# Kernel tuning notes

Measured on AMD Instinct MI355X. Metric: run time of the kernel, lower is better.

Reference implementation:

```python
import jax, jax.numpy as jnp
import numpy as np

N = 8192   # samples
D = 128    # number of variables / towers (dims[0])
D1 = 128   # hidden width (dims[1])


def setup_inputs() -> dict:
    key = jax.random.key(0)
    k_x, k_w0, k_w1, k_b1 = jax.random.split(key, 4)
    x = jax.random.normal(k_x, (N, D), dtype=jnp.float32)
    # Layer 0: one Linear(D -> D1) per tower -> batched weight [D_towers, D1, D_in]
    W0 = jax.random.normal(k_w0, (D, D1, D), dtype=jnp.float32) * (1.0 / np.sqrt(D))
    # NOTEARS init: zero self-edge column i of tower i, zero layer-0 biases
    idx = jnp.arange(D)
    W0 = W0.at[idx, :, idx].set(0.0)
    b0 = jnp.zeros((D, D1), dtype=jnp.float32)
    # Layer 1: Linear(D1 -> 1) per tower
    W1 = jax.random.normal(k_w1, (D, 1, D1), dtype=jnp.float32) * (1.0 / np.sqrt(D1))
    b1 = jax.random.normal(k_b1, (D, 1), dtype=jnp.float32) * 0.05
    return {"x": x, "W0": W0, "b0": b0, "W1": W1, "b1": b1}


def reference(x, W0, b0, W1, b1):
    # binary-input check from the original forward
    binary = jnp.all((x == 0) | (x == 1))
    # Layer 0 for all D towers at once: [n,d] x [k,h,d] -> [n,k,h]
    h = jax.nn.sigmoid(jnp.einsum('nd,khd->nkh', x, W0) + b0)
    # Layer 1 (output dim 1 per tower): [n,k,h] x [k,h] -> [n,k]
    out = jnp.einsum('nkh,kh->nk', h, W1[:, 0, :]) + b1[:, 0]
    out = jnp.where(binary, jax.nn.sigmoid(out), out)
    return out
```

## Files before the change

kernel.cpp:

```cpp
#include <hip/hip_runtime.h>
#include <hip/hip_bf16.h>
#include <stdint.h>

#define N_SAMP 8192
#define D_TOW  128
#define D_HID  128

typedef __bf16 bf16x8 __attribute__((ext_vector_type(8)));
typedef float  f32x4  __attribute__((ext_vector_type(4)));

__device__ __forceinline__ ushort f2bf(float f) {
  union { float f; uint32_t u; } c; c.f = f;
  uint32_t u = c.u;
  return (ushort)((u + 0x7FFFu + ((u >> 16) & 1u)) >> 16);
}

__device__ __forceinline__ float fast_sigmoid(float p) {
  float e = __builtin_amdgcn_exp2f(p * -1.442695040888963f);
  return __builtin_amdgcn_rcpf(1.0f + e);
}

__global__ __launch_bounds__(256) void prep_kernel(
    const float* __restrict__ x, const float* __restrict__ w0,
    ushort* __restrict__ xb, ushort* __restrict__ w0b, int* __restrict__ flag) {
  const int NX4 = (N_SAMP * D_TOW) / 4;
  const int NW4 = (D_TOW * D_HID * D_TOW) / 4;
  int t = blockIdx.x * blockDim.x + threadIdx.x;
  if (t < NX4) {
    float4 v = ((const float4*)x)[t];
    bool bad = !(((v.x == 0.f) || (v.x == 1.f)) &&
                 ((v.y == 0.f) || (v.y == 1.f)) &&
                 ((v.z == 0.f) || (v.z == 1.f)) &&
                 ((v.w == 0.f) || (v.w == 1.f)));
    ushort4 o;
    o.x = f2bf(v.x); o.y = f2bf(v.y); o.z = f2bf(v.z); o.w = f2bf(v.w);
    ((ushort4*)xb)[t] = o;
    if (__ballot(bad) != 0ull && (threadIdx.x & 63) == 0) *flag = 1;
  } else if (t < NX4 + NW4) {
    int j = t - NX4;
    float4 v = ((const float4*)w0)[j];
    ushort4 o;
    o.x = f2bf(v.x); o.y = f2bf(v.y); o.z = f2bf(v.z); o.w = f2bf(v.w);
    ((ushort4*)w0b)[j] = o;
  }
}

__device__ __forceinline__ void g2l16(const void* g, void* l) {
  __builtin_amdgcn_global_load_lds(
      (const __attribute__((address_space(1))) void*)g,
      (__attribute__((address_space(3))) void*)l, 16, 0, 0);
}

__global__ __launch_bounds__(256, 2) void towers_kernel(
    const ushort* __restrict__ xb, const ushort* __restrict__ w0b,
    const float* __restrict__ b0, const float* __restrict__ w1,
    const float* __restrict__ b1, const int* __restrict__ flag,
    float* __restrict__ out) {
  __shared__ __align__(16) ushort sX[128 * 128];
  __shared__ __align__(16) ushort sW[128 * 128];
  __shared__ float sRed[128][2];

  int bid = blockIdx.x;
  int xcd = bid & 7;
  int idx = bid >> 3;
  int k = xcd * 16 + (idx >> 6);
  int n0 = (idx & 63) * 128;

  int tid = threadIdx.x;
  int lane = tid & 63;
  int wave = tid >> 6;
  int q = lane >> 4;
  int cl = lane & 15;

  const ushort* xg = xb + n0 * 128;
  const ushort* wg = w0b + k * (128 * 128);

#pragma unroll
  for (int i = 0; i < 8; ++i) {
    int base = wave * 8192 + i * 1024;
    int row = wave * 32 + i * 4 + q;
    int c = cl ^ (row & 15);
    int off = row * 128 + c * 8;
    g2l16(xg + off, (char*)sX + base);
    g2l16(wg + off, (char*)sW + base);
  }
  __syncthreads();

  int R  = (wave >> 1) * 64;
  int Ch = (wave & 1) * 64;

  f32x4 acc[4][4];
#pragma unroll
  for (int hf = 0; hf < 4; ++hf)
#pragma unroll
    for (int nf = 0; nf < 4; ++nf)
      acc[hf][nf] = (f32x4){0.f, 0.f, 0.f, 0.f};

  int aBase[4], bBase[4];
#pragma unroll
  for (int f = 0; f < 4; ++f) {
    aBase[f] = (Ch + f * 16 + cl) * 256;
    bBase[f] = (R + f * 16 + cl) * 256;
  }

#pragma unroll
  for (int t = 0; t < 4; ++t) {
    int ch = ((t * 4 + q) ^ cl) << 4;
    bf16x8 a[4], b[4];
#pragma unroll
    for (int hf = 0; hf < 4; ++hf)
      a[hf] = *(const bf16x8*)((const char*)sW + aBase[hf] + ch);
#pragma unroll
    for (int nf = 0; nf < 4; ++nf)
      b[nf] = *(const bf16x8*)((const char*)sX + bBase[nf] + ch);
#pragma unroll
    for (int hf = 0; hf < 4; ++hf)
#pragma unroll
      for (int nf = 0; nf < 4; ++nf)
        acc[hf][nf] = __builtin_amdgcn_mfma_f32_16x16x32_bf16(
            a[hf], b[nf], acc[hf][nf], 0, 0, 0);
  }

  f32x4 bb[4], wv[4];
#pragma unroll
  for (int hf = 0; hf < 4; ++hf) {
    int h = k * 128 + Ch + hf * 16 + q * 4;
    bb[hf] = *(const f32x4*)&b0[h];
    wv[hf] = *(const f32x4*)&w1[h];
  }
  float s[4] = {0.f, 0.f, 0.f, 0.f};
#pragma unroll
  for (int hf = 0; hf < 4; ++hf)
#pragma unroll
    for (int nf = 0; nf < 4; ++nf)
#pragma unroll
      for (int r = 0; r < 4; ++r)
        s[nf] += wv[hf][r] * fast_sigmoid(acc[hf][nf][r] + bb[hf][r]);

#pragma unroll
  for (int m = 16; m <= 32; m <<= 1)
#pragma unroll
    for (int nf = 0; nf < 4; ++nf)
      s[nf] += __shfl_xor(s[nf], m, 64);

  if (q == 0) {
#pragma unroll
    for (int nf = 0; nf < 4; ++nf)
      sRed[R + nf * 16 + cl][wave & 1] = s[nf];
  }
  __syncthreads();

  if (tid < 128) {
    float v = sRed[tid][0] + sRed[tid][1] + b1[k];
    if (*flag == 0) v = fast_sigmoid(v);
    out[(size_t)(n0 + tid) * D_TOW + k] = v;
  }
}

extern "C" void kernel_launch(void* const* d_in, const int* in_sizes, int n_in,
                              void* d_out, int out_size, void* d_ws, size_t ws_size,
                              hipStream_t stream) {
  const float* x  = (const float*)d_in[0];
  const float* w0 = (const float*)d_in[1];
  const float* b0 = (const float*)d_in[2];
  const float* w1 = (const float*)d_in[3];
  const float* b1 = (const float*)d_in[4];
  float* out = (float*)d_out;

  char* ws = (char*)d_ws;
  int* flag = (int*)ws;
  ushort* xb  = (ushort*)(ws + 1024);
  ushort* w0b = (ushort*)(ws + 1024 + N_SAMP * D_TOW * 2);

  hipMemsetAsync(flag, 0, 4, stream);

  int total4 = (N_SAMP * D_TOW + D_TOW * D_HID * D_TOW) / 4;
  prep_kernel<<<total4 / 256, 256, 0, stream>>>(x, w0, xb, w0b, flag);

  towers_kernel<<<8192, 256, 0, stream>>>(xb, w0b, b0, w1, b1, flag, out);
}
```

Baseline: 138.0 us.

## Drop X LDS staging, raise occupancy, fold exp scale into weights, per-block flags

The tower kernel no longer stages x tiles in LDS. It reads B fragments straight from global memory, which halves shared memory use, and launch bounds are raised to 4 blocks per SIMD. The -log2(e) factor is folded into W0 during bf16 conversion and into b0, and the sigmoid now shares one reciprocal across each pair of values. The binary check writes a flag per block instead of using a memset plus one global flag, removing a launch, and the tile order now iterates k fastest for W reuse. In exchange, the direct global loads of x may be less efficient, and the pair-shared reciprocal slightly changes the numerics.

```diff
diff --git a/kernel.cpp b/kernel.cpp
--- a/kernel.cpp
+++ b/kernel.cpp
@@ -22,11 +22,15 @@
 
 __global__ __launch_bounds__(256) void prep_kernel(
     const float* __restrict__ x, const float* __restrict__ w0,
-    ushort* __restrict__ xb, ushort* __restrict__ w0b, int* __restrict__ flag) {
+    ushort* __restrict__ xb, ushort* __restrict__ w0b,
+    int* __restrict__ flagArr) {
   const int NX4 = (N_SAMP * D_TOW) / 4;
-  const int NW4 = (D_TOW * D_HID * D_TOW) / 4;
-  int t = blockIdx.x * blockDim.x + threadIdx.x;
-  if (t < NX4) {
+  int bid = blockIdx.x;
+  int tid = threadIdx.x;
+  int t = bid * 256 + tid;
+  if (bid < 1024) {
+    __shared__ int sbad;
+    if (tid == 0) sbad = 0;
     float4 v = ((const float4*)x)[t];
     bool bad = !(((v.x == 0.f) || (v.x == 1.f)) &&
                  ((v.y == 0.f) || (v.y == 1.f)) &&
@@ -35,12 +39,17 @@
     ushort4 o;
     o.x = f2bf(v.x); o.y = f2bf(v.y); o.z = f2bf(v.z); o.w = f2bf(v.w);
     ((ushort4*)xb)[t] = o;
-    if (__ballot(bad) != 0ull && (threadIdx.x & 63) == 0) *flag = 1;
-  } else if (t < NX4 + NW4) {
+    __syncthreads();
+    if (__ballot(bad) != 0ull && (tid & 63) == 0) sbad = 1;
+    __syncthreads();
+    if (tid == 0) flagArr[bid] = sbad;
+  } else {
+    const float c = -1.442695040888963f;
     int j = t - NX4;
     float4 v = ((const float4*)w0)[j];
     ushort4 o;
-    o.x = f2bf(v.x); o.y = f2bf(v.y); o.z = f2bf(v.z); o.w = f2bf(v.w);
+    o.x = f2bf(c * v.x); o.y = f2bf(c * v.y);
+    o.z = f2bf(c * v.z); o.w = f2bf(c * v.w);
     ((ushort4*)w0b)[j] = o;
   }
 }
@@ -51,20 +60,20 @@
       (__attribute__((address_space(3))) void*)l, 16, 0, 0);
 }
 
-__global__ __launch_bounds__(256, 2) void towers_kernel(
+__global__ __launch_bounds__(256, 4) void towers_kernel(
     const ushort* __restrict__ xb, const ushort* __restrict__ w0b,
     const float* __restrict__ b0, const float* __restrict__ w1,
-    const float* __restrict__ b1, const int* __restrict__ flag,
+    const float* __restrict__ b1, const int* __restrict__ flagArr,
     float* __restrict__ out) {
-  __shared__ __align__(16) ushort sX[128 * 128];
   __shared__ __align__(16) ushort sW[128 * 128];
   __shared__ float sRed[128][2];
+  __shared__ int sBadW[4];
 
   int bid = blockIdx.x;
   int xcd = bid & 7;
   int idx = bid >> 3;
-  int k = xcd * 16 + (idx >> 6);
-  int n0 = (idx & 63) * 128;
+  int k  = xcd * 16 + (idx & 15);
+  int n0 = (idx >> 4) * 128;
 
   int tid = threadIdx.x;
   int lane = tid & 63;
@@ -72,7 +81,6 @@
   int q = lane >> 4;
   int cl = lane & 15;
 
-  const ushort* xg = xb + n0 * 128;
   const ushort* wg = w0b + k * (128 * 128);
 
 #pragma unroll
@@ -80,10 +88,14 @@
     int base = wave * 8192 + i * 1024;
     int row = wave * 32 + i * 4 + q;
     int c = cl ^ (row & 15);
-    int off = row * 128 + c * 8;
-    g2l16(xg + off, (char*)sX + base);
-    g2l16(wg + off, (char*)sW + base);
-  }
+    g2l16(wg + row * 128 + c * 8, (char*)sW + base);
+  }
+
+  int4 fv = ((const int4*)flagArr)[tid];
+  int anyb = fv.x | fv.y | fv.z | fv.w;
+  unsigned long long mb = __ballot(anyb != 0);
+  if (lane == 0) sBadW[wave] = (mb != 0ull) ? 1 : 0;
+
   __syncthreads();
 
   int R  = (wave >> 1) * 64;
@@ -96,23 +108,24 @@
     for (int nf = 0; nf < 4; ++nf)
       acc[hf][nf] = (f32x4){0.f, 0.f, 0.f, 0.f};
 
-  int aBase[4], bBase[4];
+  int aBase[4], bOff[4];
+  const char* xgc = (const char*)(xb + n0 * 128);
 #pragma unroll
   for (int f = 0; f < 4; ++f) {
     aBase[f] = (Ch + f * 16 + cl) * 256;
-    bBase[f] = (R + f * 16 + cl) * 256;
+    bOff[f]  = (R + f * 16 + cl) * 256 + q * 16;
   }
 
 #pragma unroll
   for (int t = 0; t < 4; ++t) {
+    bf16x8 a[4], b[4];
+#pragma unroll
+    for (int nf = 0; nf < 4; ++nf)
+      b[nf] = *(const bf16x8*)(xgc + bOff[nf] + t * 64);
     int ch = ((t * 4 + q) ^ cl) << 4;
-    bf16x8 a[4], b[4];
 #pragma unroll
     for (int hf = 0; hf < 4; ++hf)
       a[hf] = *(const bf16x8*)((const char*)sW + aBase[hf] + ch);
-#pragma unroll
-    for (int nf = 0; nf < 4; ++nf)
-      b[nf] = *(const bf16x8*)((const char*)sX + bBase[nf] + ch);
 #pragma unroll
     for (int hf = 0; hf < 4; ++hf)
 #pragma unroll
@@ -121,21 +134,31 @@
             a[hf], b[nf], acc[hf][nf], 0, 0, 0);
   }
 
-  f32x4 bb[4], wv[4];
+  f32x4 bbs[4], wv[4];
 #pragma unroll
   for (int hf = 0; hf < 4; ++hf) {
     int h = k * 128 + Ch + hf * 16 + q * 4;
-    bb[hf] = *(const f32x4*)&b0[h];
+    f32x4 b0v = *(const f32x4*)&b0[h];
     wv[hf] = *(const f32x4*)&w1[h];
+    bbs[hf] = b0v * -1.442695040888963f;
   }
   float s[4] = {0.f, 0.f, 0.f, 0.f};
 #pragma unroll
   for (int hf = 0; hf < 4; ++hf)
 #pragma unroll
-    for (int nf = 0; nf < 4; ++nf)
-#pragma unroll
-      for (int r = 0; r < 4; ++r)
-        s[nf] += wv[hf][r] * fast_sigmoid(acc[hf][nf][r] + bb[hf][r]);
+    for (int nf = 0; nf < 4; ++nf) {
+      f32x4 qv = acc[hf][nf] + bbs[hf];
+      float d0 = 1.0f + __builtin_amdgcn_exp2f(qv[0]);
+      float d1 = 1.0f + __builtin_amdgcn_exp2f(qv[1]);
+      float d2 = 1.0f + __builtin_amdgcn_exp2f(qv[2]);
+      float d3 = 1.0f + __builtin_amdgcn_exp2f(qv[3]);
+      float r01 = __builtin_amdgcn_rcpf(d0 * d1);
+      float r23 = __builtin_amdgcn_rcpf(d2 * d3);
+      s[nf] += wv[hf][0] * (r01 * d1);
+      s[nf] += wv[hf][1] * (r01 * d0);
+      s[nf] += wv[hf][2] * (r23 * d3);
+      s[nf] += wv[hf][3] * (r23 * d2);
+    }
 
 #pragma unroll
   for (int m = 16; m <= 32; m <<= 1)
@@ -151,8 +174,9 @@
   __syncthreads();
 
   if (tid < 128) {
+    int anyBad = sBadW[0] | sBadW[1] | sBadW[2] | sBadW[3];
     float v = sRed[tid][0] + sRed[tid][1] + b1[k];
-    if (*flag == 0) v = fast_sigmoid(v);
+    if (anyBad == 0) v = fast_sigmoid(v);
     out[(size_t)(n0 + tid) * D_TOW + k] = v;
   }
 }
@@ -168,14 +192,12 @@
   float* out = (float*)d_out;
 
   char* ws = (char*)d_ws;
-  int* flag = (int*)ws;
-  ushort* xb  = (ushort*)(ws + 1024);
-  ushort* w0b = (ushort*)(ws + 1024 + N_SAMP * D_TOW * 2);
-
-  hipMemsetAsync(flag, 0, 4, stream);
+  int* flagArr = (int*)ws;
+  ushort* xb  = (ushort*)(ws + 4096);
+  ushort* w0b = (ushort*)(ws + 4096 + N_SAMP * D_TOW * 2);
 
   int total4 = (N_SAMP * D_TOW + D_TOW * D_HID * D_TOW) / 4;
-  prep_kernel<<<total4 / 256, 256, 0, stream>>>(x, w0, xb, w0b, flag);
-
-  towers_kernel<<<8192, 256, 0, stream>>>(xb, w0b, b0, w1, b1, flag, out);
-}
+  prep_kernel<<<total4 / 256, 256, 0, stream>>>(x, w0, xb, w0b, flagArr);
+
+  towers_kernel<<<8192, 256, 0, stream>>>(xb, w0b, b0, w1, b1, flagArr, out);
+}
```

Measured after the change: 157.1 us. 1.14x slower.
